# Performance work log

Measured on AMD Instinct MI355X. Metric: run time of the kernel, lower is better.

## Reference

```python
import jax, jax.numpy as jnp
import numpy as np

TAU = 2.0
BN_EPS = 1e-5
HEADS = 8

# spikingjelly-style Heaviside spike with sigmoid surrogate gradient (alpha=4)
@jax.custom_vjp
def spike(x):
    return (x >= 0.0).astype(x.dtype)

def _spike_fwd(x):
    return (x >= 0.0).astype(x.dtype), x

def _spike_bwd(x, g):
    s = jax.nn.sigmoid(4.0 * x)
    return (g * 4.0 * s * (1.0 - s),)

spike.defvjp(_spike_fwd, _spike_bwd)

def lif(x, thresh):
    """Multi-step LIF (tau=2, decay_input=True, hard reset to 0, detach_reset).
    x: (T, ...) input current; returns spikes of the same shape."""
    def step(v, xt):
        v = v + (xt - v) / TAU          # charge
        s = spike(v - thresh)           # fire
        v = v * (1.0 - jax.lax.stop_gradient(s))  # hard reset, detached
        return v, s
    _, s = jax.lax.scan(step, jnp.zeros_like(x[0]), x)
    return s

def bn(x, gamma, beta, mean, var):
    # inference-mode BatchNorm2d over channel axis 2 of (T,B,C,H,W)
    sh = (1, 1, -1, 1, 1)
    scale = gamma / jnp.sqrt(var + BN_EPS)
    return (x - mean.reshape(sh)) * scale.reshape(sh) + beta.reshape(sh)

def setup_inputs() -> dict:
    key = jax.random.key(0)
    T, B, C, H, W = 4, 16, 512, 16, 16
    ks = jax.random.split(key, 24)
    def wmat(k):
        return jax.random.normal(k, (C, C), jnp.float32) * (1.0 / np.sqrt(C))
    def bnp(k):
        k1, k2, k3, k4 = jax.random.split(k, 4)
        return (jax.random.normal(k1, (C,), jnp.float32) * 0.1 + 1.0,
                jax.random.normal(k2, (C,), jnp.float32) * 0.1,
                jax.random.normal(k3, (C,), jnp.float32) * 0.1,
                jax.random.uniform(k4, (C,), jnp.float32) + 0.5)
    qg, qb, qm, qvar = bnp(ks[1]); kg, kb, km, kvar = bnp(ks[3])
    vg, vb, vm, vvar = bnp(ks[5]); pg, pb, pm, pvar = bnp(ks[8])
    return {
        'x': jax.random.normal(ks[0], (T, B, C, H, W), jnp.float32),
        'wq': wmat(ks[10]), 'qg': qg, 'qb': qb, 'qm': qm, 'qvar': qvar,
        'wk': wmat(ks[11]), 'kg': kg, 'kb': kb, 'km': km, 'kvar': kvar,
        'wv': wmat(ks[12]), 'vg': vg, 'vb': vb, 'vm': vm, 'vvar': vvar,
        'wp': wmat(ks[13]), 'bp': jax.random.normal(ks[14], (C,), jnp.float32) * 0.02,
        'pg': pg, 'pb': pb, 'pm': pm, 'pvar': pvar,
    }

def reference(x, wq, qg, qb, qm, qvar, wk, kg, kb, km, kvar,
              wv, vg, vb, vm, vvar, wp, bp, pg, pb, pm, pvar):
    T, B, C, H, W = x.shape
    dh = C // HEADS
    N = H * W
    identity = x
    xs = lif(x, 1.0)  # shortcut_lif

    def branch(w, g, b, m, v):
        y = jnp.einsum('tbchw,oc->tbohw', xs, w)  # 1x1 conv, no bias
        return lif(bn(y, g, b, m, v), 1.0)

    # (T,B,C,H,W) spikes -> (T,B,heads,N,dh)
    def to_heads(s):
        return s.reshape(T, B, HEADS, dh, N).transpose(0, 1, 2, 4, 3)

    q = to_heads(branch(wq, qg, qb, qm, qvar))
    k = to_heads(branch(wk, kg, kb, km, kvar))
    v = to_heads(branch(wv, vg, vb, vm, vvar))

    kv = (k * v).sum(axis=3, keepdims=True)   # sum over tokens N -> (T,B,h,1,dh)
    kv = lif(kv, 0.5)                          # talking_heads_lif (v_threshold=0.5)

    out = q * kv                               # (T,B,h,N,dh)
    out = out.transpose(0, 1, 2, 4, 3).reshape(T, B, C, H, W)
    out = jnp.einsum('tbchw,oc->tbohw', out, wp) + bp.reshape(1, 1, -1, 1, 1)
    out = bn(out, pg, pb, pm, pvar) + identity
    return out, v
```

## Files before the change

kernel.cpp:

```cpp
#include <hip/hip_runtime.h>
#include <hip/hip_bf16.h>

typedef unsigned short u16;
typedef unsigned int u32;
typedef __attribute__((ext_vector_type(8))) short bh8;
typedef __attribute__((ext_vector_type(4))) short sh4;
typedef __attribute__((ext_vector_type(4))) float f4;

#define T_   4
#define B_   16
#define C_   512
#define N_   256
#define M2_  4096

__device__ __forceinline__ u16 f2bf(float f) {
  u32 u = __float_as_uint(f);
  u32 r = (u + 0x7FFFu + ((u >> 16) & 1u)) >> 16;
  return (u16)r;
}
__device__ __forceinline__ void gl_lds16(const void* g, void* l) {
  __builtin_amdgcn_global_load_lds(
      (const __attribute__((address_space(1))) unsigned int*)g,
      (__attribute__((address_space(3))) unsigned int*)l, 16, 0, 0);
}

__global__ void k_prep_lif(const float* __restrict__ x, u16* __restrict__ xs,
                           const float* __restrict__ wq, const float* __restrict__ wk,
                           const float* __restrict__ wv, const float* __restrict__ wp,
                           const float* qg, const float* qb, const float* qm, const float* qv,
                           const float* kg, const float* kb, const float* km, const float* kv2,
                           const float* vg, const float* vb, const float* vm, const float* vv,
                           const float* pg, const float* pb, const float* pm, const float* pv,
                           const float* bp,
                           u16* __restrict__ wcat, u16* __restrict__ wpcat,
                           float* bns, float* pss) {
  __shared__ u16 sp[4][64][68];
  int bid = blockIdx.x;
  int tid = threadIdx.x;
  if (bid < 512) {
    int b = bid >> 5, c0 = ((bid >> 2) & 7) * 64, n0 = (bid & 3) * 64;
    int rq = tid >> 4;
    int n4 = (tid & 15) * 4;
    f4 xr[4][4];
#pragma unroll
    for (int t = 0; t < 4; t++) {
      const float* xb = x + (((size_t)t * 16 + b) * 512 + c0) * 256 + n0;
#pragma unroll
      for (int i = 0; i < 4; i++)
        xr[t][i] = *(const f4*)(xb + (size_t)(rq + i * 16) * 256 + n4);
    }
    float v[16];
#pragma unroll
    for (int i = 0; i < 16; i++) v[i] = 0.f;
#pragma unroll
    for (int t = 0; t < 4; t++) {
#pragma unroll
      for (int i = 0; i < 4; i++) {
        int row = rq + i * 16;
        sh4 sv;
#pragma unroll
        for (int j = 0; j < 4; j++) {
          float vv2 = v[i * 4 + j];
          vv2 = vv2 + (xr[t][i][j] - vv2) * 0.5f;
          u16 s = 0;
          if (vv2 >= 1.0f) { s = 0x3F80; vv2 = 0.f; }
          v[i * 4 + j] = vv2;
          sv[j] = (short)s;
        }
        *(sh4*)&sp[t][row][n4] = sv;
      }
    }
    __syncthreads();
    int cp = (tid & 31) * 2;
    int nq = tid >> 5;
    for (int t = 0; t < 4; t++) {
      u16* ob = xs + (((size_t)t * 16 + b) * 256 + n0) * 512 + c0;
#pragma unroll
      for (int i = 0; i < 8; i++) {
        int n = nq + i * 8;
        u32 w = (u32)sp[t][cp][n] | ((u32)sp[t][cp + 1][n] << 16);
        *(u32*)(ob + (size_t)n * 512 + cp) = w;
      }
    }
  } else {
    int id = (bid - 512) * 256 + tid;
    if (id < 1048576) {
      int mat = id >> 18;
      int rc  = id & 262143;
      int o = rc >> 9, c = rc & 511;
      const float* src = (mat == 0) ? wq : (mat == 1) ? wk : (mat == 2) ? wv : wp;
      float w = src[rc];
      u16 hu = f2bf(w);
      float hf = __uint_as_float(((u32)hu) << 16);
      u16 lu = f2bf(w - hf);
      if (mat < 3) {
        int rI = (o >> 5) * 96 + mat * 32 + (o & 31);
        size_t base = (size_t)rI * 1024 + c;
        wcat[base] = hu; wcat[base + 512] = lu;
      } else {
        size_t base = (size_t)o * 1024 + c;
        wpcat[base] = hu; wpcat[base + 512] = lu;
      }
    } else {
      int j = id - 1048576;
      if (j < 1536) {
        int br = j >> 9, o = j & 511;
        const float *g, *b, *m, *va;
        if (br == 0)      { g = qg; b = qb; m = qm; va = qv; }
        else if (br == 1) { g = kg; b = kb; m = km; va = kv2; }
        else              { g = vg; b = vb; m = vm; va = vv; }
        float s = g[o] / sqrtf(va[o] + 1e-5f);
        int rI = (o >> 5) * 96 + br * 32 + (o & 31);
        bns[rI * 4 + 0] = s; bns[rI * 4 + 1] = m[o]; bns[rI * 4 + 2] = b[o];
        bns[rI * 4 + 3] = 0.f;
      } else if (j < 2048) {
        int c = j - 1536;
        float s = pg[c] / sqrtf(pv[c] + 1e-5f);
        pss[c * 4 + 0] = bp[c]; pss[c * 4 + 1] = pm[c];
        pss[c * 4 + 2] = s;     pss[c * 4 + 3] = pb[c];
      }
    }
  }
}

__launch_bounds__(256, 2)
__global__ void k_qkv_gemm(const u16* __restrict__ xs, const u16* __restrict__ wcat,
                           const float* __restrict__ bns,
                           u16* __restrict__ qs, float* __restrict__ vout,
                           int* __restrict__ kvp) {
  __shared__ char lds[81920];
  int tid = threadIdx.x, lane = tid & 63;
  int wid = tid >> 6;
  int mw = wid & 1, kw = wid >> 1;
  int lr = lane & 15, lq = lane >> 4;
  int m0 = blockIdx.x * 128;
  int cb = blockIdx.y;
  int o0 = cb * 96;
  int b = m0 >> 8, n0 = m0 & 255, half = (m0 >> 7) & 1;

  int srow = tid >> 3;
  u32 sgoff = (u32)(((tid & 7) ^ (srow & 7)) << 4);
  u32 ldst = (u32)tid * 16;

  u32 aoff[4], boff[6];
#pragma unroll
  for (int mi = 0; mi < 4; mi++) {
    int r = mw * 64 + mi * 16 + lr;
    aoff[mi] = r * 128 + (((lq ^ (r & 7)) ^ (kw << 2)) << 4);
  }
#pragma unroll
  for (int ni = 0; ni < 6; ni++) {
    int r = ni * 16 + lr;
    boff[ni] = r * 128 + (((lq ^ (r & 7)) ^ (kw << 2)) << 4);
  }

  const char* Bb = (const char*)wcat + (size_t)o0 * 2048;

  auto STAGE = [&](int buf, int step) {
    int t = step >> 3;
    u32 kb = (u32)(step & 7) * 128;
    const char* Ab = (const char*)xs + ((size_t)t * M2_ + m0) * 1024;
    char* L = lds + buf * 40960;
#pragma unroll
    for (int r2 = 0; r2 < 4; r2++)
      gl_lds16(Ab + (size_t)(r2 * 32 + srow) * 1024 + kb + sgoff, L + r2 * 4096 + ldst);
#pragma unroll
    for (int r2 = 0; r2 < 3; r2++) {
      gl_lds16(Bb + (size_t)(r2 * 32 + srow) * 2048 + kb + sgoff, L + 16384 + r2 * 4096 + ldst);
      gl_lds16(Bb + (size_t)(r2 * 32 + srow) * 2048 + 1024 + kb + sgoff, L + 28672 + r2 * 4096 + ldst);
    }
  };

  float vst[4][6][4];
#pragma unroll
  for (int a = 0; a < 4; a++)
#pragma unroll
    for (int bq = 0; bq < 6; bq++)
#pragma unroll
      for (int c = 0; c < 4; c++) vst[a][bq][c] = 0.f;

  f4 acc[4][6];
  STAGE(0, 0);
  __syncthreads();
  int cur = 0;
  for (int step = 0; step < 32; ++step) {
    int ks = step & 7;
    if (ks == 0) {
#pragma unroll
      for (int a = 0; a < 4; a++)
#pragma unroll
        for (int bq = 0; bq < 6; bq++) { acc[a][bq][0] = 0.f; acc[a][bq][1] = 0.f; acc[a][bq][2] = 0.f; acc[a][bq][3] = 0.f; }
    }
    if (step < 31) STAGE(cur ^ 1, step + 1);
    const char* L = lds + cur * 40960;
    bh8 af[4];
#pragma unroll
    for (int mi = 0; mi < 4; mi++)
      af[mi] = *(const bh8*)(L + aoff[mi]);
#pragma unroll
    for (int ni = 0; ni < 6; ni++) {
      bh8 bf = *(const bh8*)(L + 16384 + boff[ni]);
      bh8 lf = *(const bh8*)(L + 28672 + boff[ni]);
#pragma unroll
      for (int mi = 0; mi < 4; mi++)
        acc[mi][ni] = __builtin_amdgcn_mfma_f32_16x16x32_bf16(af[mi], bf, acc[mi][ni], 0, 0, 0);
#pragma unroll
      for (int mi = 0; mi < 4; mi++)
        acc[mi][ni] = __builtin_amdgcn_mfma_f32_16x16x32_bf16(af[mi], lf, acc[mi][ni], 0, 0, 0);
    }
    asm volatile("s_waitcnt vmcnt(0)" ::: "memory");
    __builtin_amdgcn_s_barrier();
    cur ^= 1;
    if (ks == 7) {
      int t = step >> 3;
      char* dead = lds + (cur ^ 1) * 40960;
#pragma unroll
      for (int p = 0; p < 2; p++) {
        if (kw == 1) {
#pragma unroll
          for (int m2 = 0; m2 < 2; m2++)
#pragma unroll
            for (int ni = 0; ni < 6; ni++)
              *(f4*)(dead + (((mw * 12 + m2 * 6 + ni) * 64 + lane) << 4)) = acc[p * 2 + m2][ni];
        }
        asm volatile("s_waitcnt lgkmcnt(0)" ::: "memory");
        __builtin_amdgcn_s_barrier();
        if (kw == 0) {
#pragma unroll
          for (int m2 = 0; m2 < 2; m2++)
#pragma unroll
            for (int ni = 0; ni < 6; ni++) {
              f4 o = *(const f4*)(dead + (((mw * 12 + m2 * 6 + ni) * 64 + lane) << 4));
              acc[p * 2 + m2][ni][0] += o[0];
              acc[p * 2 + m2][ni][1] += o[1];
              acc[p * 2 + m2][ni][2] += o[2];
              acc[p * 2 + m2][ni][3] += o[3];
            }
        }
        asm volatile("s_waitcnt lgkmcnt(0)" ::: "memory");
        __builtin_amdgcn_s_barrier();
      }
      unsigned char* vbuf = (unsigned char*)dead;
      short* cbuf = (short*)(dead + 4096);
      if (kw == 0) {
        int cnt0 = 0, cnt1 = 0;
        u16 kbits[4]; kbits[0] = 0; kbits[1] = 0; kbits[2] = 0; kbits[3] = 0;
#pragma unroll
        for (int ni = 0; ni < 6; ni++) {
          int rI = o0 + ni * 16 + lr;
          f4 bn4 = *(const f4*)&bns[rI * 4];
          int jj = ni & 1;
#pragma unroll
          for (int mi = 0; mi < 4; mi++) {
#pragma unroll
            for (int j = 0; j < 4; j++) {
              float y = (acc[mi][ni][j] - bn4[1]) * bn4[0] + bn4[2];
              float vv = vst[mi][ni][j];
              vv = vv + (y - vv) * 0.5f;
              int s = (vv >= 1.0f) ? 1 : 0;
              if (s) vv = 0.f;
              vst[mi][ni][j] = vv;
              if (ni < 2) {
                int rg = m0 + mw * 64 + mi * 16 + lq * 4 + j;
                int cc = cb * 32 + jj * 16 + lr;
                qs[((size_t)t * M2_ + rg) * 512 + cc] = s ? (u16)0x3F80 : (u16)0;
              } else if (ni < 4) {
                kbits[mi] |= (u16)(s << (jj * 4 + j));
              } else {
                int row = mw * 64 + mi * 16 + lq * 4 + j;
                vbuf[row * 32 + jj * 16 + lr] = (unsigned char)s;
                int kbit = (kbits[mi] >> (jj * 4 + j)) & 1;
                if (jj == 0) cnt0 += (s & kbit); else cnt1 += (s & kbit);
              }
            }
          }
        }
        cbuf[tid * 2] = (short)cnt0; cbuf[tid * 2 + 1] = (short)cnt1;
      }
      asm volatile("s_waitcnt lgkmcnt(0)" ::: "memory");
      __builtin_amdgcn_s_barrier();
      {
        int d0 = (cb & 1) * 32;
        int hh = cb >> 1;
        float* vo = vout + (((size_t)(t * 16 + b) * 8 + hh) * 256 + n0) * 64 + d0;
#pragma unroll
        for (int p = 0; p < 4; p++) {
          int row = (tid >> 3) + p * 32;
          const unsigned char* src = vbuf + row * 32 + (tid & 7) * 4;
          f4 w2; w2[0] = src[0]; w2[1] = src[1]; w2[2] = src[2]; w2[3] = src[3];
          *(f4*)(vo + (size_t)row * 64 + (tid & 7) * 4) = w2;
        }
        if (tid < 32) {
          int lr2 = tid & 15, jj = tid >> 4;
          int ssum = 0;
#pragma unroll
          for (int w3 = 0; w3 < 2; w3++)
#pragma unroll
            for (int q3 = 0; q3 < 4; q3++)
              ssum += cbuf[(w3 * 64 + q3 * 16 + lr2) * 2 + jj];
          kvp[(((t * 16 + b) * 2 + half) << 9) + cb * 32 + jj * 16 + lr2] = ssum;
        }
      }
      asm volatile("s_waitcnt lgkmcnt(0)" ::: "memory");
      __builtin_amdgcn_s_barrier();
    }
  }
}

__launch_bounds__(256, 2)
__global__ void k_proj_gemm(const u16* __restrict__ qs, const int* __restrict__ kvp,
                            const u16* __restrict__ wpc, const float* __restrict__ pss,
                            const float* __restrict__ x, float* __restrict__ out) {
  __shared__ char lds[66560];
  u16* lm = (u16*)(lds + 65536);
  int tid = threadIdx.x, lane = tid & 63, wid = tid >> 6;
  int wr = wid >> 1, wc = wid & 1, lr = lane & 15, lq = lane >> 4;
  int m0 = blockIdx.x * 128, o0 = blockIdx.y * 64;
  int tb = m0 >> 8;

  {
    int b_ = tb & 15, tt = tb >> 4;
#pragma unroll
    for (int ci = 0; ci < 2; ci++) {
      int cc = tid + ci * 256;
      float v = 0.f; u16 mk = 0;
#pragma unroll
      for (int t2 = 0; t2 < 4; t2++) {
        int tb2 = t2 * 16 + b_;
        int s = kvp[((tb2 * 2) << 9) + cc] + kvp[((tb2 * 2 + 1) << 9) + cc];
        v = v + ((float)s - v) * 0.5f;
        int sp = (v >= 0.5f) ? 1 : 0;
        if (sp) v = 0.f;
        if (t2 == tt) mk = sp ? (u16)0xFFFF : (u16)0;
      }
      lm[cc] = mk;
    }
  }

  int srow = tid >> 3;
  u32 sgoff = (u32)(((tid & 7) ^ (srow & 7)) << 4);
  u32 ldst = (u32)tid * 16;

  u32 aoff[4], boff[2];
#pragma unroll
  for (int mi = 0; mi < 4; mi++) {
    int r = wr * 64 + mi * 16 + lr;
    aoff[mi] = r * 128 + ((lq ^ (r & 7)) << 4);
  }
#pragma unroll
  for (int ni = 0; ni < 2; ni++) {
    int r = wc * 32 + ni * 16 + lr;
    boff[ni] = r * 128 + ((lq ^ (r & 7)) << 4);
  }

  const char* Ab = (const char*)qs + (size_t)m0 * 1024;
  const char* Bb = (const char*)wpc + (size_t)o0 * 2048;

  auto STAGE = [&](int buf, int step) {
    u32 kb = (u32)step * 128;
    char* L = lds + buf * 32768;
#pragma unroll
    for (int r2 = 0; r2 < 4; r2++)
      gl_lds16(Ab + (size_t)(r2 * 32 + srow) * 1024 + kb + sgoff, L + r2 * 4096 + ldst);
#pragma unroll
    for (int r2 = 0; r2 < 2; r2++) {
      gl_lds16(Bb + (size_t)(r2 * 32 + srow) * 2048 + kb + sgoff, L + 16384 + r2 * 4096 + ldst);
      gl_lds16(Bb + (size_t)(r2 * 32 + srow) * 2048 + 1024 + kb + sgoff, L + 24576 + r2 * 4096 + ldst);
    }
  };

  f4 acc[4][2];
#pragma unroll
  for (int a = 0; a < 4; a++)
#pragma unroll
    for (int b2 = 0; b2 < 2; b2++) { acc[a][b2][0] = 0.f; acc[a][b2][1] = 0.f; acc[a][b2][2] = 0.f; acc[a][b2][3] = 0.f; }

  STAGE(0, 0);
  __syncthreads();
  int cur = 0;
  for (int step = 0; step < 8; ++step) {
    u32 kb = (u32)step * 128;
    if (step < 7) STAGE(cur ^ 1, step + 1);
    const char* L = lds + cur * 32768;
#pragma unroll
    for (int h = 0; h < 2; h++) {
      u32 hx = (u32)h << 6;
      bh8 mq = *(const bh8*)((const char*)lm + kb + (h << 6) + lq * 16);
      bh8 af[4], bf[2], lf[2];
#pragma unroll
      for (int mi = 0; mi < 4; mi++) {
        af[mi] = *(const bh8*)(L + (aoff[mi] ^ hx));
        af[mi] = af[mi] & mq;
      }
#pragma unroll
      for (int ni = 0; ni < 2; ni++) {
        bf[ni] = *(const bh8*)(L + 16384 + (boff[ni] ^ hx));
        lf[ni] = *(const bh8*)(L + 24576 + (boff[ni] ^ hx));
      }
#pragma unroll
      for (int mi = 0; mi < 4; mi++)
#pragma unroll
        for (int ni = 0; ni < 2; ni++)
          acc[mi][ni] = __builtin_amdgcn_mfma_f32_16x16x32_bf16(af[mi], bf[ni], acc[mi][ni], 0, 0, 0);
#pragma unroll
      for (int mi = 0; mi < 4; mi++)
#pragma unroll
        for (int ni = 0; ni < 2; ni++)
          acc[mi][ni] = __builtin_amdgcn_mfma_f32_16x16x32_bf16(af[mi], lf[ni], acc[mi][ni], 0, 0, 0);
    }
    asm volatile("s_waitcnt vmcnt(0)" ::: "memory");
    __builtin_amdgcn_s_barrier();
    cur ^= 1;
  }
#pragma unroll
  for (int mi = 0; mi < 4; mi++)
#pragma unroll
    for (int ni = 0; ni < 2; ni++) {
      int o = o0 + wc * 32 + ni * 16 + lr;
      f4 ps = *(const f4*)&pss[o * 4];
      int n = (m0 & 255) + wr * 64 + mi * 16 + lq * 4;
      size_t idx = (size_t)tb * 131072 + (size_t)o * 256 + n;
      f4 xv = *(const f4*)&x[idx];
      f4 res;
#pragma unroll
      for (int j = 0; j < 4; j++) {
        float u = acc[mi][ni][j] + ps[0];
        u = (u - ps[1]) * ps[2] + ps[3];
        res[j] = u + xv[j];
      }
      *(f4*)&out[idx] = res;
    }
}

extern "C" void kernel_launch(void* const* d_in, const int* in_sizes, int n_in,
                              void* d_out, int out_size, void* d_ws, size_t ws_size,
                              hipStream_t stream) {
  const float* x  = (const float*)d_in[0];
  const float* wq = (const float*)d_in[1];
  const float* qg = (const float*)d_in[2];
  const float* qb = (const float*)d_in[3];
  const float* qm = (const float*)d_in[4];
  const float* qv = (const float*)d_in[5];
  const float* wk = (const float*)d_in[6];
  const float* kg = (const float*)d_in[7];
  const float* kb = (const float*)d_in[8];
  const float* km = (const float*)d_in[9];
  const float* kv = (const float*)d_in[10];
  const float* wv = (const float*)d_in[11];
  const float* vg = (const float*)d_in[12];
  const float* vb = (const float*)d_in[13];
  const float* vm = (const float*)d_in[14];
  const float* vv = (const float*)d_in[15];
  const float* wp = (const float*)d_in[16];
  const float* bp = (const float*)d_in[17];
  const float* pg = (const float*)d_in[18];
  const float* pb = (const float*)d_in[19];
  const float* pm = (const float*)d_in[20];
  const float* pv = (const float*)d_in[21];

  char* w = (char*)d_ws;
  u16*  XS    = (u16*)(w + 0);
  u16*  QS    = (u16*)(w + 16777216);
  u16*  WCAT  = (u16*)(w + 33554432);
  u16*  WPCAT = (u16*)(w + 36700160);
  float* BNS  = (float*)(w + 37748736);
  float* PSS  = (float*)(w + 37773312);
  int*   KVP  = (int*)(w + 37781504);

  float* out  = (float*)d_out;
  float* vout = out + 8388608;

  k_prep_lif<<<4616, 256, 0, stream>>>(x, XS, wq, wk, wv, wp,
                                       qg, qb, qm, qv, kg, kb, km, kv,
                                       vg, vb, vm, vv, pg, pb, pm, pv, bp,
                                       WCAT, WPCAT, BNS, PSS);
  k_qkv_gemm<<<dim3(32, 16), 256, 0, stream>>>(XS, WCAT, BNS, QS, vout, KVP);
  k_proj_gemm<<<dim3(128, 8), 256, 0, stream>>>(QS, KVP, WPCAT, PSS, x, out);
}
```

Measured before the change: 239.1 us.

## Split QKV GEMM warps over output columns instead of K halves

The four waves of the fused QKV GEMM now split the output columns, each wave owning half the 16-column tiles, instead of splitting the K dimension in two halves. Each wave loops over both K halves itself. This removes the LDS cross-wave reduction and its extra barriers at the end of each time step. The BN and LIF epilogue now runs on all four waves rather than two, and the BN constants are hoisted into registers before the loop. The cost is that each wave reads the full K range from LDS per step and performs twice as many MFMAs per step on half the accumulator tiles.

Result: faster. 198.2 us (-17.1%).

```diff
diff --git a/kernel.cpp b/kernel.cpp
--- a/kernel.cpp
+++ b/kernel.cpp
@@ -131,27 +131,34 @@
   __shared__ char lds[81920];
   int tid = threadIdx.x, lane = tid & 63;
   int wid = tid >> 6;
-  int mw = wid & 1, kw = wid >> 1;
+  int mw = wid & 1, wn = wid >> 1;
   int lr = lane & 15, lq = lane >> 4;
   int m0 = blockIdx.x * 128;
   int cb = blockIdx.y;
   int o0 = cb * 96;
   int b = m0 >> 8, n0 = m0 & 255, half = (m0 >> 7) & 1;
 
+  float scl[3], mn[3], bt[3];
+#pragma unroll
+  for (int ni = 0; ni < 3; ni++) {
+    int rI = o0 + (ni * 2 + wn) * 16 + lr;
+    scl[ni] = bns[rI * 4]; mn[ni] = bns[rI * 4 + 1]; bt[ni] = bns[rI * 4 + 2];
+  }
+
   int srow = tid >> 3;
   u32 sgoff = (u32)(((tid & 7) ^ (srow & 7)) << 4);
   u32 ldst = (u32)tid * 16;
 
-  u32 aoff[4], boff[6];
+  u32 aoff[4], boff[3];
 #pragma unroll
   for (int mi = 0; mi < 4; mi++) {
     int r = mw * 64 + mi * 16 + lr;
-    aoff[mi] = r * 128 + (((lq ^ (r & 7)) ^ (kw << 2)) << 4);
-  }
-#pragma unroll
-  for (int ni = 0; ni < 6; ni++) {
-    int r = ni * 16 + lr;
-    boff[ni] = r * 128 + (((lq ^ (r & 7)) ^ (kw << 2)) << 4);
+    aoff[mi] = r * 128 + ((lq ^ (r & 7)) << 4);
+  }
+#pragma unroll
+  for (int ni = 0; ni < 3; ni++) {
+    int r = (ni * 2 + wn) * 16 + lr;
+    boff[ni] = r * 128 + ((lq ^ (r & 7)) << 4);
   }
 
   const char* Bb = (const char*)wcat + (size_t)o0 * 2048;
@@ -171,15 +178,15 @@
     }
   };
 
-  float vst[4][6][4];
+  float vst[4][3][4];
 #pragma unroll
   for (int a = 0; a < 4; a++)
 #pragma unroll
-    for (int bq = 0; bq < 6; bq++)
+    for (int bq = 0; bq < 3; bq++)
 #pragma unroll
       for (int c = 0; c < 4; c++) vst[a][bq][c] = 0.f;
 
-  f4 acc[4][6];
+  f4 acc[4][3];
   STAGE(0, 0);
   __syncthreads();
   int cur = 0;
@@ -189,24 +196,32 @@
 #pragma unroll
       for (int a = 0; a < 4; a++)
 #pragma unroll
-        for (int bq = 0; bq < 6; bq++) { acc[a][bq][0] = 0.f; acc[a][bq][1] = 0.f; acc[a][bq][2] = 0.f; acc[a][bq][3] = 0.f; }
+        for (int bq = 0; bq < 3; bq++) { acc[a][bq][0] = 0.f; acc[a][bq][1] = 0.f; acc[a][bq][2] = 0.f; acc[a][bq][3] = 0.f; }
     }
     if (step < 31) STAGE(cur ^ 1, step + 1);
     const char* L = lds + cur * 40960;
-    bh8 af[4];
-#pragma unroll
-    for (int mi = 0; mi < 4; mi++)
-      af[mi] = *(const bh8*)(L + aoff[mi]);
-#pragma unroll
-    for (int ni = 0; ni < 6; ni++) {
-      bh8 bf = *(const bh8*)(L + 16384 + boff[ni]);
-      bh8 lf = *(const bh8*)(L + 28672 + boff[ni]);
+#pragma unroll
+    for (int h = 0; h < 2; h++) {
+      u32 hx = (u32)h << 6;
+      bh8 af[4], bf[3], lf[3];
 #pragma unroll
       for (int mi = 0; mi < 4; mi++)
-        acc[mi][ni] = __builtin_amdgcn_mfma_f32_16x16x32_bf16(af[mi], bf, acc[mi][ni], 0, 0, 0);
+        af[mi] = *(const bh8*)(L + (aoff[mi] ^ hx));
+#pragma unroll
+      for (int ni = 0; ni < 3; ni++) {
+        bf[ni] = *(const bh8*)(L + 16384 + (boff[ni] ^ hx));
+        lf[ni] = *(const bh8*)(L + 28672 + (boff[ni] ^ hx));
+      }
 #pragma unroll
       for (int mi = 0; mi < 4; mi++)
-        acc[mi][ni] = __builtin_amdgcn_mfma_f32_16x16x32_bf16(af[mi], lf, acc[mi][ni], 0, 0, 0);
+#pragma unroll
+        for (int ni = 0; ni < 3; ni++)
+          acc[mi][ni] = __builtin_amdgcn_mfma_f32_16x16x32_bf16(af[mi], bf[ni], acc[mi][ni], 0, 0, 0);
+#pragma unroll
+      for (int mi = 0; mi < 4; mi++)
+#pragma unroll
+        for (int ni = 0; ni < 3; ni++)
+          acc[mi][ni] = __builtin_amdgcn_mfma_f32_16x16x32_bf16(af[mi], lf[ni], acc[mi][ni], 0, 0, 0);
     }
     asm volatile("s_waitcnt vmcnt(0)" ::: "memory");
     __builtin_amdgcn_s_barrier();
@@ -214,69 +229,36 @@
     if (ks == 7) {
       int t = step >> 3;
       char* dead = lds + (cur ^ 1) * 40960;
-#pragma unroll
-      for (int p = 0; p < 2; p++) {
-        if (kw == 1) {
-#pragma unroll
-          for (int m2 = 0; m2 < 2; m2++)
-#pragma unroll
-            for (int ni = 0; ni < 6; ni++)
-              *(f4*)(dead + (((mw * 12 + m2 * 6 + ni) * 64 + lane) << 4)) = acc[p * 2 + m2][ni];
-        }
-        asm volatile("s_waitcnt lgkmcnt(0)" ::: "memory");
-        __builtin_amdgcn_s_barrier();
-        if (kw == 0) {
-#pragma unroll
-          for (int m2 = 0; m2 < 2; m2++)
-#pragma unroll
-            for (int ni = 0; ni < 6; ni++) {
-              f4 o = *(const f4*)(dead + (((mw * 12 + m2 * 6 + ni) * 64 + lane) << 4));
-              acc[p * 2 + m2][ni][0] += o[0];
-              acc[p * 2 + m2][ni][1] += o[1];
-              acc[p * 2 + m2][ni][2] += o[2];
-              acc[p * 2 + m2][ni][3] += o[3];
-            }
-        }
-        asm volatile("s_waitcnt lgkmcnt(0)" ::: "memory");
-        __builtin_amdgcn_s_barrier();
-      }
       unsigned char* vbuf = (unsigned char*)dead;
       short* cbuf = (short*)(dead + 4096);
-      if (kw == 0) {
-        int cnt0 = 0, cnt1 = 0;
-        u16 kbits[4]; kbits[0] = 0; kbits[1] = 0; kbits[2] = 0; kbits[3] = 0;
-#pragma unroll
-        for (int ni = 0; ni < 6; ni++) {
-          int rI = o0 + ni * 16 + lr;
-          f4 bn4 = *(const f4*)&bns[rI * 4];
-          int jj = ni & 1;
-#pragma unroll
-          for (int mi = 0; mi < 4; mi++) {
-#pragma unroll
-            for (int j = 0; j < 4; j++) {
-              float y = (acc[mi][ni][j] - bn4[1]) * bn4[0] + bn4[2];
-              float vv = vst[mi][ni][j];
-              vv = vv + (y - vv) * 0.5f;
-              int s = (vv >= 1.0f) ? 1 : 0;
-              if (s) vv = 0.f;
-              vst[mi][ni][j] = vv;
-              if (ni < 2) {
-                int rg = m0 + mw * 64 + mi * 16 + lq * 4 + j;
-                int cc = cb * 32 + jj * 16 + lr;
-                qs[((size_t)t * M2_ + rg) * 512 + cc] = s ? (u16)0x3F80 : (u16)0;
-              } else if (ni < 4) {
-                kbits[mi] |= (u16)(s << (jj * 4 + j));
-              } else {
-                int row = mw * 64 + mi * 16 + lq * 4 + j;
-                vbuf[row * 32 + jj * 16 + lr] = (unsigned char)s;
-                int kbit = (kbits[mi] >> (jj * 4 + j)) & 1;
-                if (jj == 0) cnt0 += (s & kbit); else cnt1 += (s & kbit);
-              }
+      int cnt = 0;
+      u32 kbits = 0;
+#pragma unroll
+      for (int ni = 0; ni < 3; ni++) {
+#pragma unroll
+        for (int mi = 0; mi < 4; mi++) {
+#pragma unroll
+          for (int j = 0; j < 4; j++) {
+            float y = (acc[mi][ni][j] - mn[ni]) * scl[ni] + bt[ni];
+            float vv = vst[mi][ni][j];
+            vv = vv + (y - vv) * 0.5f;
+            int s = (vv >= 1.0f) ? 1 : 0;
+            if (s) vv = 0.f;
+            vst[mi][ni][j] = vv;
+            if (ni == 0) {
+              int rg = m0 + mw * 64 + mi * 16 + lq * 4 + j;
+              qs[((size_t)t * M2_ + rg) * 512 + cb * 32 + wn * 16 + lr] = s ? (u16)0x3F80 : (u16)0;
+            } else if (ni == 1) {
+              kbits |= (u32)s << (mi * 4 + j);
+            } else {
+              int row = mw * 64 + mi * 16 + lq * 4 + j;
+              vbuf[row * 32 + wn * 16 + lr] = (unsigned char)s;
+              cnt += s & (int)((kbits >> (mi * 4 + j)) & 1);
             }
           }
         }
-        cbuf[tid * 2] = (short)cnt0; cbuf[tid * 2 + 1] = (short)cnt1;
-      }
+      }
+      cbuf[tid] = (short)cnt;
       asm volatile("s_waitcnt lgkmcnt(0)" ::: "memory");
       __builtin_amdgcn_s_barrier();
       {
@@ -291,14 +273,14 @@
           *(f4*)(vo + (size_t)row * 64 + (tid & 7) * 4) = w2;
         }
         if (tid < 32) {
-          int lr2 = tid & 15, jj = tid >> 4;
+          int lr2 = tid & 15, wn2 = tid >> 4;
           int ssum = 0;
 #pragma unroll
-          for (int w3 = 0; w3 < 2; w3++)
-#pragma unroll
-            for (int q3 = 0; q3 < 4; q3++)
-              ssum += cbuf[(w3 * 64 + q3 * 16 + lr2) * 2 + jj];
-          kvp[(((t * 16 + b) * 2 + half) << 9) + cb * 32 + jj * 16 + lr2] = ssum;
+          for (int mw2 = 0; mw2 < 2; mw2++)
+#pragma unroll
+            for (int lq2 = 0; lq2 < 4; lq2++)
+              ssum += cbuf[((wn2 * 2 + mw2) << 6) + lq2 * 16 + lr2];
+          kvp[(((t * 16 + b) * 2 + half) << 9) + cb * 32 + wn2 * 16 + lr2] = ssum;
         }
       }
       asm volatile("s_waitcnt lgkmcnt(0)" ::: "memory");
```
